# Performance work log

Hardware: AMD Instinct MI355X
Metric: run time of the kernel (lower is better)

Reference implementation:

```python
import jax, jax.numpy as jnp
import numpy as np

B, T, N, F, E, L = 2, 2, 10000, 128, 160000, 2


def setup_inputs() -> dict:
    key = jax.random.key(0)
    k = jax.random.split(key, 6)
    feature = jax.random.normal(k[0], (B, T, N, F), jnp.float32)
    edge_src = jax.random.randint(k[1], (E,), 0, N, jnp.int32)
    edge_dst = jax.random.randint(k[2], (E,), 0, N, jnp.int32)
    s = 1.0 / np.sqrt(F).astype(np.float32)
    W_self = jax.random.normal(k[3], (L, F, F), jnp.float32) * s
    W_neigh = jax.random.normal(k[4], (L, F, F), jnp.float32) * s
    b = jnp.zeros((L, F), jnp.float32)
    return dict(feature=feature, W_self=W_self, W_neigh=W_neigh, b=b,
                edge_src=edge_src, edge_dst=edge_dst)


def reference(feature, W_self, W_neigh, b, edge_src, edge_dst):
    # feature: [B, T, N, Fin]; edge (src -> dst) as in dgl.from_scipy(csr).
    Bs, Ts, Ns, Fin = feature.shape
    num_layers = W_self.shape[0]
    # in-degree per dst node; mean over zero in-degree nodes is 0 (DGL semantics)
    deg = jax.ops.segment_sum(jnp.ones(edge_dst.shape, jnp.float32), edge_dst,
                              num_segments=Ns)
    inv_deg = jnp.where(deg > 0, 1.0 / jnp.maximum(deg, 1.0), 0.0)  # [N]
    # node-major layout for gather/scatter: [N, B, T, F]
    h = jnp.transpose(feature, (2, 0, 1, 3))
    for l in range(num_layers):
        msg = h[edge_src]  # [E, B, T, F] irregular gather
        agg = jax.ops.segment_sum(msg, edge_dst, num_segments=Ns)
        h_neigh = agg * inv_deg[:, None, None, None]  # mean aggregation
        h = (jnp.einsum('nbtf,fg->nbtg', h, W_self[l])
             + jnp.einsum('nbtf,fg->nbtg', h_neigh, W_neigh[l])
             + b[l])
    # res.permute(0,2,1,3) in torch -> [B, T, N, Fout]
    return jnp.transpose(h, (1, 2, 0, 3))
```

## Files before the change

kernel.cpp:

```cpp
#include <hip/hip_runtime.h>

constexpr int N_  = 10000;
constexpr int F_  = 128;
constexpr int E_  = 160000;
constexpr int BT_ = 4;
constexpr int M_  = N_ * BT_;
constexpr int CAP = 64;

typedef __attribute__((ext_vector_type(8))) short bf16x8;
typedef __attribute__((ext_vector_type(4))) float f32x4;
typedef __attribute__((ext_vector_type(8))) unsigned short u16x8;

static __device__ inline float bf2f(unsigned short u) {
    union { unsigned int i; float f; } v; v.i = ((unsigned int)u) << 16; return v.f;
}
static __device__ inline unsigned short f2bf(float f) {
    union { float f; unsigned int i; } v; v.f = f;
    unsigned int x = v.i;
    return (unsigned short)((x + 0x7fffu + ((x >> 16) & 1u)) >> 16);
}


__global__ __launch_bounds__(256) void k_pre(const float4* __restrict__ feat,
        unsigned short* __restrict__ h0, const int* __restrict__ src,
        const int* __restrict__ dst, int* __restrict__ cursor,
        int* __restrict__ bucket, const float* __restrict__ Wself,
        const float* __restrict__ Wneigh, unsigned short* __restrict__ Wp) {
    const int b = blockIdx.x;
    const int tid = threadIdx.x;
    if (b < 625) {
        int e = b * 256 + tid;
        if (e < E_) {
            int d = dst[e];
            int p = atomicAdd(&cursor[d], 1);
            if (p < CAP) bucket[d * CAP + p] = src[e];
        }
    } else if (b < 657) {
        int t = (b - 625) * 256 + tid;
        int mat = t >> 11;
        int r = t & 2047;
        int kb = r >> 9;
        int nb = (r >> 6) & 7;
        int lane = r & 63;
        int l = mat >> 1, s = mat & 1;
        const float* W = (s ? Wneigh : Wself) + (size_t)l * F_ * F_;
        int k0 = kb * 32 + (lane >> 4) * 8;
        int n  = nb * 16 + (lane & 15);
        unsigned short* dstp = Wp + (size_t)mat * 16384 +
                               (size_t)((kb * 8 + nb) * 64 + lane) * 8;
#pragma unroll
        for (int j = 0; j < 8; j++) dstp[j] = f2bf(W[(size_t)(k0 + j) * F_ + n]);
    } else {
        int i = (b - 657) * 256 + tid;
        int f4 = i & 31;
        int m  = i >> 5;
        int n  = m >> 2;
        int bt = m & 3;
        float4 v = feat[(bt * N_ + n) * 32 + f4];
        ushort4 o;
        o.x = f2bf(v.x); o.y = f2bf(v.y); o.z = f2bf(v.z); o.w = f2bf(v.w);
        *(ushort4*)(h0 + (size_t)m * 128 + f4 * 4) = o;
    }
}


template <bool LAST>
__global__ __launch_bounds__(256) void k_fused(const unsigned short* __restrict__ h,
        const int* __restrict__ cursor, const int* __restrict__ bucket,
        const unsigned short* __restrict__ Wp, const float* __restrict__ bias,
        void* __restrict__ outv) {
    __shared__ unsigned short aggs[4][4][4][136];
    const int tid  = threadIdx.x;
    const int wave = tid >> 6, lane = tid & 63;
    const int m0   = blockIdx.x * 64 + wave * 16;
    const int node0 = m0 >> 2;
    const int col  = lane & 15;
    const int quad = lane >> 4;

#pragma unroll
    for (int nl = 0; nl < 4; nl++) {
        const int n = node0 + nl;
        const int deg = cursor[n];
        const int nn = deg < CAP ? deg : CAP;
        float acc[8] = {0, 0, 0, 0, 0, 0, 0, 0};
        int idx = bucket[n * CAP + (lane < nn ? lane : 0)];
#pragma unroll 4
        for (int e = 0; e < nn; e++) {
            int s = __builtin_amdgcn_readlane(idx, e);
            u16x8 a = *(const u16x8*)(h + (size_t)s * 512 + lane * 8);
#pragma unroll
            for (int j = 0; j < 8; j++) acc[j] += bf2f(a[j]);
        }
        float w = (deg > 0) ? 1.0f / (float)deg : 0.0f;
        u16x8 o;
#pragma unroll
        for (int j = 0; j < 8; j++) o[j] = f2bf(acc[j] * w);
        *(u16x8*)&aggs[wave][nl][lane >> 4][(lane & 15) * 8] = o;
    }
    __syncthreads();

    f32x4 acc[8];
#pragma unroll
    for (int nb = 0; nb < 8; nb++) {
        float b = bias[nb * 16 + col];
        acc[nb] = (f32x4){b, b, b, b};
    }

    const unsigned short* A0 = h + (size_t)(m0 + col) * 128 + quad * 8;
    const unsigned short* As = &aggs[wave][col >> 2][col & 3][quad * 8];
    const unsigned short* B0 = Wp + (size_t)lane * 8;
    const unsigned short* B1 = B0 + 16384;

#pragma unroll
    for (int kb = 0; kb < 4; kb++) {
        bf16x8 a = *(const bf16x8*)(A0 + kb * 32);
#pragma unroll
        for (int nb = 0; nb < 8; nb++) {
            bf16x8 b = *(const bf16x8*)(B0 + (size_t)((kb * 8 + nb) * 64) * 8);
            acc[nb] = __builtin_amdgcn_mfma_f32_16x16x32_bf16(a, b, acc[nb], 0, 0, 0);
        }
    }
#pragma unroll
    for (int kb = 0; kb < 4; kb++) {
        bf16x8 a = *(const bf16x8*)(As + kb * 32);
#pragma unroll
        for (int nb = 0; nb < 8; nb++) {
            bf16x8 b = *(const bf16x8*)(B1 + (size_t)((kb * 8 + nb) * 64) * 8);
            acc[nb] = __builtin_amdgcn_mfma_f32_16x16x32_bf16(a, b, acc[nb], 0, 0, 0);
        }
    }

    if (LAST) {
        float* out = (float*)outv;
#pragma unroll
        for (int nb = 0; nb < 8; nb++) {
#pragma unroll
            for (int r = 0; r < 4; r++) {
                int m = m0 + quad * 4 + r;
                int node = m >> 2, bt = m & 3;
                out[((size_t)bt * N_ + node) * 128 + nb * 16 + col] = acc[nb][r];
            }
        }
    } else {
        unsigned short* out = (unsigned short*)outv;
#pragma unroll
        for (int nb = 0; nb < 8; nb++) {
#pragma unroll
            for (int r = 0; r < 4; r++) {
                int m = m0 + quad * 4 + r;
                out[(size_t)m * 128 + nb * 16 + col] = f2bf(acc[nb][r]);
            }
        }
    }
}


extern "C" void kernel_launch(void* const* d_in, const int* in_sizes, int n_in,
                              void* d_out, int out_size, void* d_ws, size_t ws_size,
                              hipStream_t stream) {
    const float* feature = (const float*)d_in[0];
    const float* W_self  = (const float*)d_in[1];
    const float* W_neigh = (const float*)d_in[2];
    const float* bias    = (const float*)d_in[3];
    const int*   e_src   = (const int*)d_in[4];
    const int*   e_dst   = (const int*)d_in[5];
    float*       out     = (float*)d_out;

    char* ws = (char*)d_ws;
    unsigned short* h0   = (unsigned short*)ws;  ws += (size_t)M_ * F_ * 2;
    unsigned short* h1   = (unsigned short*)ws;  ws += (size_t)M_ * F_ * 2;
    unsigned short* Wp   = (unsigned short*)ws;  ws += (size_t)4 * 16384 * 2;
    int*   cursor  = (int*)ws;                   ws += (size_t)N_ * 4;
    int*   bucket  = (int*)ws;                   ws += (size_t)N_ * CAP * 4;

    hipMemsetAsync(cursor, 0, (size_t)N_ * 4, stream);

    k_pre<<<5657, 256, 0, stream>>>((const float4*)feature, h0, e_src, e_dst,
                                    cursor, bucket, W_self, W_neigh, Wp);

    const int gb = M_ / 64;
    k_fused<false><<<gb, 256, 0, stream>>>(h0, cursor, bucket, Wp, bias, h1);
    k_fused<true><<<gb, 256, 0, stream>>>(h1, cursor, bucket, Wp + 2 * 16384,
                                          bias + F_, out);
}
```

Measured before the change: 172.0 us.

## Merge three kernels into one persistent kernel with grid barriers and dynamic tiles

Replaces the preprocessing kernel and the two per-layer fused kernels with a single persistent kernel of 512 blocks. Stages are separated by a software grid barrier built on atomics. Within each layer, waves take 16-row tiles dynamically from an atomic counter, and the per-block __syncthreads between aggregation and MFMA is removed. This targets kernel launch gaps and load imbalance, but adds spin-wait barrier cost, relies on all 512 blocks being co-resident without a cooperative launch, and runs the preprocessing at lower parallelism.

```diff
diff --git a/kernel.cpp b/kernel.cpp
--- a/kernel.cpp
+++ b/kernel.cpp
@@ -6,6 +6,8 @@
 constexpr int BT_ = 4;
 constexpr int M_  = N_ * BT_;
 constexpr int CAP = 64;
+constexpr int WT_ = 2500;
+constexpr int GRID = 512;
 
 typedef __attribute__((ext_vector_type(8))) short bf16x8;
 typedef __attribute__((ext_vector_type(4))) float f32x4;
@@ -20,137 +22,167 @@
     return (unsigned short)((x + 0x7fffu + ((x >> 16) & 1u)) >> 16);
 }
 
-
-__global__ __launch_bounds__(256) void k_pre(const float4* __restrict__ feat,
-        unsigned short* __restrict__ h0, const int* __restrict__ src,
-        const int* __restrict__ dst, int* __restrict__ cursor,
-        int* __restrict__ bucket, const float* __restrict__ Wself,
-        const float* __restrict__ Wneigh, unsigned short* __restrict__ Wp) {
-    const int b = blockIdx.x;
+static __device__ inline void gridbar(int* __restrict__ cnt, int* __restrict__ gen) {
+    __syncthreads();
+    if (threadIdx.x == 0) {
+        __threadfence();
+        int g = __hip_atomic_load(gen, __ATOMIC_RELAXED, __HIP_MEMORY_SCOPE_AGENT);
+        int v = __hip_atomic_fetch_add(cnt, 1, __ATOMIC_ACQ_REL, __HIP_MEMORY_SCOPE_AGENT);
+        if (v == GRID - 1) {
+            __hip_atomic_store(cnt, 0, __ATOMIC_RELAXED, __HIP_MEMORY_SCOPE_AGENT);
+            __hip_atomic_fetch_add(gen, 1, __ATOMIC_ACQ_REL, __HIP_MEMORY_SCOPE_AGENT);
+        } else {
+            while (__hip_atomic_load(gen, __ATOMIC_RELAXED,
+                                     __HIP_MEMORY_SCOPE_AGENT) == g)
+                __builtin_amdgcn_s_sleep(2);
+        }
+        __threadfence();
+    }
+    __syncthreads();
+}
+
+
+__global__ __launch_bounds__(256, 2) void k_mega(
+        const float4* __restrict__ feat, const int* __restrict__ src,
+        const int* __restrict__ dst, const float* __restrict__ Wself,
+        const float* __restrict__ Wneigh, const float* __restrict__ bias,
+        unsigned short* __restrict__ h0, unsigned short* __restrict__ h1,
+        unsigned short* __restrict__ Wp, int* __restrict__ cursor,
+        int* __restrict__ bucket, int* __restrict__ ctrl,
+        float* __restrict__ out) {
     const int tid = threadIdx.x;
-    if (b < 625) {
-        int e = b * 256 + tid;
-        if (e < E_) {
+    const int blk = blockIdx.x;
+
+    for (int c = blk; c < 5657; c += GRID) {
+        if (c < 625) {
+            int e = c * 256 + tid;
             int d = dst[e];
             int p = atomicAdd(&cursor[d], 1);
             if (p < CAP) bucket[d * CAP + p] = src[e];
+        } else if (c < 657) {
+            int t = (c - 625) * 256 + tid;
+            int mat = t >> 11;
+            int r = t & 2047;
+            int kb = r >> 9;
+            int nb = (r >> 6) & 7;
+            int lane = r & 63;
+            int l = mat >> 1, s = mat & 1;
+            const float* W = (s ? Wneigh : Wself) + (size_t)l * F_ * F_;
+            int k0 = kb * 32 + (lane >> 4) * 8;
+            int n  = nb * 16 + (lane & 15);
+            unsigned short* dstp = Wp + (size_t)mat * 16384 +
+                                   (size_t)((kb * 8 + nb) * 64 + lane) * 8;
+#pragma unroll
+            for (int j = 0; j < 8; j++) dstp[j] = f2bf(W[(size_t)(k0 + j) * F_ + n]);
+        } else {
+            int i = (c - 657) * 256 + tid;
+            int f4 = i & 31;
+            int m  = i >> 5;
+            int n  = m >> 2;
+            int bt = m & 3;
+            float4 v = feat[(bt * N_ + n) * 32 + f4];
+            ushort4 o;
+            o.x = f2bf(v.x); o.y = f2bf(v.y); o.z = f2bf(v.z); o.w = f2bf(v.w);
+            *(ushort4*)(h0 + (size_t)m * 128 + f4 * 4) = o;
         }
-    } else if (b < 657) {
-        int t = (b - 625) * 256 + tid;
-        int mat = t >> 11;
-        int r = t & 2047;
-        int kb = r >> 9;
-        int nb = (r >> 6) & 7;
-        int lane = r & 63;
-        int l = mat >> 1, s = mat & 1;
-        const float* W = (s ? Wneigh : Wself) + (size_t)l * F_ * F_;
-        int k0 = kb * 32 + (lane >> 4) * 8;
-        int n  = nb * 16 + (lane & 15);
-        unsigned short* dstp = Wp + (size_t)mat * 16384 +
-                               (size_t)((kb * 8 + nb) * 64 + lane) * 8;
-#pragma unroll
-        for (int j = 0; j < 8; j++) dstp[j] = f2bf(W[(size_t)(k0 + j) * F_ + n]);
-    } else {
-        int i = (b - 657) * 256 + tid;
-        int f4 = i & 31;
-        int m  = i >> 5;
-        int n  = m >> 2;
-        int bt = m & 3;
-        float4 v = feat[(bt * N_ + n) * 32 + f4];
-        ushort4 o;
-        o.x = f2bf(v.x); o.y = f2bf(v.y); o.z = f2bf(v.z); o.w = f2bf(v.w);
-        *(ushort4*)(h0 + (size_t)m * 128 + f4 * 4) = o;
     }
-}
-
-
-template <bool LAST>
-__global__ __launch_bounds__(256) void k_fused(const unsigned short* __restrict__ h,
-        const int* __restrict__ cursor, const int* __restrict__ bucket,
-        const unsigned short* __restrict__ Wp, const float* __restrict__ bias,
-        void* __restrict__ outv) {
+    gridbar(ctrl, ctrl + 1);
+
     __shared__ unsigned short aggs[4][4][4][136];
-    const int tid  = threadIdx.x;
     const int wave = tid >> 6, lane = tid & 63;
-    const int m0   = blockIdx.x * 64 + wave * 16;
-    const int node0 = m0 >> 2;
     const int col  = lane & 15;
     const int quad = lane >> 4;
 
-#pragma unroll
-    for (int nl = 0; nl < 4; nl++) {
-        const int n = node0 + nl;
-        const int deg = cursor[n];
-        const int nn = deg < CAP ? deg : CAP;
-        float acc[8] = {0, 0, 0, 0, 0, 0, 0, 0};
-        int idx = bucket[n * CAP + (lane < nn ? lane : 0)];
-#pragma unroll 4
-        for (int e = 0; e < nn; e++) {
-            int s = __builtin_amdgcn_readlane(idx, e);
-            u16x8 a = *(const u16x8*)(h + (size_t)s * 512 + lane * 8);
-#pragma unroll
-            for (int j = 0; j < 8; j++) acc[j] += bf2f(a[j]);
+    for (int l = 0; l < 2; l++) {
+        const unsigned short* hin = l ? h1 : h0;
+        const unsigned short* B0  = Wp + (size_t)l * 2 * 16384 + (size_t)lane * 8;
+        const unsigned short* B1  = B0 + 16384;
+        const float* bL = bias + l * F_;
+        int* wc = ctrl + 2 + l;
+
+        for (;;) {
+            int wt;
+            if (lane == 0)
+                wt = __hip_atomic_fetch_add(wc, 1, __ATOMIC_RELAXED,
+                                            __HIP_MEMORY_SCOPE_AGENT);
+            wt = __builtin_amdgcn_readfirstlane(wt);
+            if (wt >= WT_) break;
+
+            const int m0 = wt * 16;
+            const int node0 = m0 >> 2;
+
+#pragma unroll
+            for (int nl = 0; nl < 4; nl++) {
+                const int n = node0 + nl;
+                const int deg = cursor[n];
+                const int nn = deg < CAP ? deg : CAP;
+                float acc[8] = {0, 0, 0, 0, 0, 0, 0, 0};
+                int idx = bucket[n * CAP + (lane < nn ? lane : 0)];
+#pragma unroll 8
+                for (int e = 0; e < nn; e++) {
+                    int s = __builtin_amdgcn_readlane(idx, e);
+                    u16x8 a = *(const u16x8*)(hin + (size_t)s * 512 + lane * 8);
+#pragma unroll
+                    for (int j = 0; j < 8; j++) acc[j] += bf2f(a[j]);
+                }
+                float w = (deg > 0) ? 1.0f / (float)deg : 0.0f;
+                u16x8 o;
+#pragma unroll
+                for (int j = 0; j < 8; j++) o[j] = f2bf(acc[j] * w);
+                *(u16x8*)&aggs[wave][nl][lane >> 4][(lane & 15) * 8] = o;
+            }
+
+            f32x4 acc[8];
+#pragma unroll
+            for (int nb = 0; nb < 8; nb++) {
+                float b = bL[nb * 16 + col];
+                acc[nb] = (f32x4){b, b, b, b};
+            }
+
+            const unsigned short* A0 = hin + (size_t)(m0 + col) * 128 + quad * 8;
+            const unsigned short* As = &aggs[wave][col >> 2][col & 3][quad * 8];
+
+#pragma unroll
+            for (int kb = 0; kb < 4; kb++) {
+                bf16x8 a = *(const bf16x8*)(A0 + kb * 32);
+#pragma unroll
+                for (int nb = 0; nb < 8; nb++) {
+                    bf16x8 b = *(const bf16x8*)(B0 + (size_t)((kb * 8 + nb) * 64) * 8);
+                    acc[nb] = __builtin_amdgcn_mfma_f32_16x16x32_bf16(a, b, acc[nb], 0, 0, 0);
+                }
+            }
+#pragma unroll
+            for (int kb = 0; kb < 4; kb++) {
+                bf16x8 a = *(const bf16x8*)(As + kb * 32);
+#pragma unroll
+                for (int nb = 0; nb < 8; nb++) {
+                    bf16x8 b = *(const bf16x8*)(B1 + (size_t)((kb * 8 + nb) * 64) * 8);
+                    acc[nb] = __builtin_amdgcn_mfma_f32_16x16x32_bf16(a, b, acc[nb], 0, 0, 0);
+                }
+            }
+
+            if (l == 0) {
+#pragma unroll
+                for (int nb = 0; nb < 8; nb++) {
+#pragma unroll
+                    for (int r = 0; r < 4; r++) {
+                        int m = m0 + quad * 4 + r;
+                        h1[(size_t)m * 128 + nb * 16 + col] = f2bf(acc[nb][r]);
+                    }
+                }
+            } else {
+#pragma unroll
+                for (int nb = 0; nb < 8; nb++) {
+#pragma unroll
+                    for (int r = 0; r < 4; r++) {
+                        int m = m0 + quad * 4 + r;
+                        int node = m >> 2, bt = m & 3;
+                        out[((size_t)bt * N_ + node) * 128 + nb * 16 + col] = acc[nb][r];
+                    }
+                }
+            }
         }
-        float w = (deg > 0) ? 1.0f / (float)deg : 0.0f;
-        u16x8 o;
-#pragma unroll
-        for (int j = 0; j < 8; j++) o[j] = f2bf(acc[j] * w);
-        *(u16x8*)&aggs[wave][nl][lane >> 4][(lane & 15) * 8] = o;
-    }
-    __syncthreads();
-
-    f32x4 acc[8];
-#pragma unroll
-    for (int nb = 0; nb < 8; nb++) {
-        float b = bias[nb * 16 + col];
-        acc[nb] = (f32x4){b, b, b, b};
-    }
-
-    const unsigned short* A0 = h + (size_t)(m0 + col) * 128 + quad * 8;
-    const unsigned short* As = &aggs[wave][col >> 2][col & 3][quad * 8];
-    const unsigned short* B0 = Wp + (size_t)lane * 8;
-    const unsigned short* B1 = B0 + 16384;
-
-#pragma unroll
-    for (int kb = 0; kb < 4; kb++) {
-        bf16x8 a = *(const bf16x8*)(A0 + kb * 32);
-#pragma unroll
-        for (int nb = 0; nb < 8; nb++) {
-            bf16x8 b = *(const bf16x8*)(B0 + (size_t)((kb * 8 + nb) * 64) * 8);
-            acc[nb] = __builtin_amdgcn_mfma_f32_16x16x32_bf16(a, b, acc[nb], 0, 0, 0);
-        }
-    }
-#pragma unroll
-    for (int kb = 0; kb < 4; kb++) {
-        bf16x8 a = *(const bf16x8*)(As + kb * 32);
-#pragma unroll
-        for (int nb = 0; nb < 8; nb++) {
-            bf16x8 b = *(const bf16x8*)(B1 + (size_t)((kb * 8 + nb) * 64) * 8);
-            acc[nb] = __builtin_amdgcn_mfma_f32_16x16x32_bf16(a, b, acc[nb], 0, 0, 0);
-        }
-    }
-
-    if (LAST) {
-        float* out = (float*)outv;
-#pragma unroll
-        for (int nb = 0; nb < 8; nb++) {
-#pragma unroll
-            for (int r = 0; r < 4; r++) {
-                int m = m0 + quad * 4 + r;
-                int node = m >> 2, bt = m & 3;
-                out[((size_t)bt * N_ + node) * 128 + nb * 16 + col] = acc[nb][r];
-            }
-        }
-    } else {
-        unsigned short* out = (unsigned short*)outv;
-#pragma unroll
-        for (int nb = 0; nb < 8; nb++) {
-#pragma unroll
-            for (int r = 0; r < 4; r++) {
-                int m = m0 + quad * 4 + r;
-                out[(size_t)m * 128 + nb * 16 + col] = f2bf(acc[nb][r]);
-            }
-        }
+        if (l == 0) gridbar(ctrl, ctrl + 1);
     }
 }
 
@@ -158,28 +190,24 @@
 extern "C" void kernel_launch(void* const* d_in, const int* in_sizes, int n_in,
                               void* d_out, int out_size, void* d_ws, size_t ws_size,
                               hipStream_t stream) {
-    const float* feature = (const float*)d_in[0];
-    const float* W_self  = (const float*)d_in[1];
-    const float* W_neigh = (const float*)d_in[2];
-    const float* bias    = (const float*)d_in[3];
-    const int*   e_src   = (const int*)d_in[4];
-    const int*   e_dst   = (const int*)d_in[5];
-    float*       out     = (float*)d_out;
+    const float4* feature = (const float4*)d_in[0];
+    const float*  W_self  = (const float*)d_in[1];
+    const float*  W_neigh = (const float*)d_in[2];
+    const float*  bias    = (const float*)d_in[3];
+    const int*    e_src   = (const int*)d_in[4];
+    const int*    e_dst   = (const int*)d_in[5];
+    float*        out     = (float*)d_out;
 
     char* ws = (char*)d_ws;
     unsigned short* h0   = (unsigned short*)ws;  ws += (size_t)M_ * F_ * 2;
     unsigned short* h1   = (unsigned short*)ws;  ws += (size_t)M_ * F_ * 2;
     unsigned short* Wp   = (unsigned short*)ws;  ws += (size_t)4 * 16384 * 2;
     int*   cursor  = (int*)ws;                   ws += (size_t)N_ * 4;
+    int*   ctrl    = (int*)ws;                   ws += 4 * 4;
     int*   bucket  = (int*)ws;                   ws += (size_t)N_ * CAP * 4;
 
-    hipMemsetAsync(cursor, 0, (size_t)N_ * 4, stream);
-
-    k_pre<<<5657, 256, 0, stream>>>((const float4*)feature, h0, e_src, e_dst,
-                                    cursor, bucket, W_self, W_neigh, Wp);
-
-    const int gb = M_ / 64;
-    k_fused<false><<<gb, 256, 0, stream>>>(h0, cursor, bucket, Wp, bias, h1);
-    k_fused<true><<<gb, 256, 0, stream>>>(h1, cursor, bucket, Wp + 2 * 16384,
-                                          bias + F_, out);
-}
+    hipMemsetAsync(cursor, 0, (size_t)N_ * 4 + 16, stream);
+
+    k_mega<<<GRID, 256, 0, stream>>>(feature, e_src, e_dst, W_self, W_neigh,
+                                     bias, h0, h1, Wp, cursor, bucket, ctrl, out);
+}
```

New measurement: 470.3 us. 2.73x slower.
